# Optimization experiments

Hardware: AMD Instinct MI355X
Metric: run time of the kernel (lower is better)

The kernel has to match this reference:

```python
import jax, jax.numpy as jnp
import numpy as np

ST_RATIO = 1.5  # slice-thickness / in-plane-resolution ratio (module init arg)


def setup_inputs() -> dict:
    key = jax.random.key(0)
    k1, k2 = jax.random.split(key)
    B, H, W, D, S = 8, 160, 160, 96, 64
    vol = jax.random.normal(k1, (B, H, W, D, 1), dtype=jnp.float32)
    # small perturbations around identity (identity row is added inside reference)
    trf = jax.random.normal(k2, (B, S, 12), dtype=jnp.float32) * 0.05
    return {"vol": vol, "trf": trf}


def _trilinear(v, loc):
    """v: [H, W, D] volume; loc: [..., 3] float sample locations (voxel coords).
    Border-clipped trilinear interpolation (as in neuron's interpn)."""
    H, W, D = v.shape
    maxs_f = jnp.asarray([H - 1, W - 1, D - 1], dtype=loc.dtype)
    loc = jnp.clip(loc, 0.0, maxs_f)
    f = jnp.floor(loc)
    d = loc - f  # fractional part, in [0, 1)
    i0 = f.astype(jnp.int32)
    i1 = jnp.minimum(i0 + 1, jnp.asarray([H - 1, W - 1, D - 1], dtype=jnp.int32))
    out = jnp.zeros(loc.shape[:-1], dtype=v.dtype)
    for cx in (0, 1):
        for cy in (0, 1):
            for cz in (0, 1):
                ix = i1[..., 0] if cx else i0[..., 0]
                iy = i1[..., 1] if cy else i0[..., 1]
                iz = i1[..., 2] if cz else i0[..., 2]
                w = ((d[..., 0] if cx else 1.0 - d[..., 0])
                     * (d[..., 1] if cy else 1.0 - d[..., 1])
                     * (d[..., 2] if cz else 1.0 - d[..., 2]))
                out = out + w * v[ix, iy, iz]
    return out


def reference(vol, trf):
    """Volume-to-slice resampling.
    vol: [B, H, W, D, 1]; trf: [B, S, 12] per-slice affine params (flattened 3x4).
    Identity row added per original: trf += eye(4)[:3, :].
    Output: [B, H, W, S, 1]."""
    B, H, W, D, _ = vol.shape
    S = trf.shape[1]
    A = trf.reshape(B, S, 3, 4) + jnp.eye(4, dtype=trf.dtype)[:3, :]  # [B,S,3,4]

    # slice-plane sampling grid: in-plane (i, j) over HxW, through-plane z = s * st_ratio
    ii, jj = jnp.meshgrid(jnp.arange(H, dtype=jnp.float32),
                          jnp.arange(W, dtype=jnp.float32), indexing="ij")
    zz = jnp.arange(S, dtype=jnp.float32) * ST_RATIO
    ones = jnp.ones((S, H, W), dtype=jnp.float32)
    grid = jnp.stack([ii[None] * ones, jj[None] * ones,
                      zz[:, None, None] * ones, ones], axis=-1)  # [S,H,W,4] homogeneous

    loc = jnp.einsum("bsij,shwj->bshwi", A, grid)  # [B,S,H,W,3] volume coords
    out = jax.vmap(_trilinear)(vol[..., 0], loc)    # [B,S,H,W]
    return jnp.transpose(out, (0, 2, 3, 1))[..., None]  # [B,H,W,S,1]
```

## Files before the change

kernel.cpp:

```cpp
#include <hip/hip_runtime.h>
#include <hip/hip_fp16.h>

#define B 8
#define H 160
#define W 160
#define D 96
#define S 64
#define ST_RATIO 1.5f

__global__ __launch_bounds__(256) void v2s_transpose(
    const float* __restrict__ vol, __half* __restrict__ volT)
{
    __shared__ float t[32][33];
    const int blk = blockIdx.x;
    const int bh  = blk / 15;
    const int rem = blk - bh * 15;
    const int wt  = rem / 3;
    const int dt  = rem - wt * 3;
    const float* in  = vol  + (size_t)bh * (W * D);
    __half*      op  = volT + (size_t)bh * (D * W);
    const int tx = threadIdx.x & 31, ty = threadIdx.x >> 5;
#pragma unroll
    for (int r = 0; r < 4; ++r) {
        const int w_ = wt * 32 + ty + 8 * r;
        const int d_ = dt * 32 + tx;
        t[ty + 8 * r][tx] = in[w_ * D + d_];
    }
    __syncthreads();
#pragma unroll
    for (int r = 0; r < 4; ++r) {
        const int d_ = dt * 32 + ty + 8 * r;
        const int w_ = wt * 32 + tx;
        op[d_ * W + w_] = __float2half(t[tx][ty + 8 * r]);
    }
}

__global__ __launch_bounds__(256) void v2s_main(
    const __half* __restrict__ volT,
    const float*  __restrict__ trf,
    float*        __restrict__ out)
{
    __shared__ float As[S * 12];
    __shared__ float outT[64][65];

    const int bid  = blockIdx.x;
    const int tile = (bid & 7) * 400 + (bid >> 3);
    const int b    = tile / 400;
    const int hw0  = (tile - b * 400) * 64;

    const float* tb = trf + (size_t)b * (S * 12);
    for (int e = threadIdx.x; e < S * 12; e += 256) {
        const int j = e % 12;
        float v = tb[e];
        if ((j & 3) == (j >> 2)) v += 1.0f;
        As[e] = v;
    }
    __syncthreads();

    const int lane = threadIdx.x & 63;
    const int wid  = threadIdx.x >> 6;
    const int hw   = hw0 + lane;
    const int h    = hw / W;
    const int w    = hw - h * W;
    const float fh = (float)h, fw = (float)w;
    const __half* vb = volT + (size_t)b * (H * D * W);

#pragma unroll 4
    for (int it = 0; it < 16; ++it) {
        const int s = it * 4 + wid;
        const float* a = &As[s * 12];
        const float fz = (float)s * ST_RATIO;

        float x = fmaf(a[0], fh, fmaf(a[1], fw, fmaf(a[2],  fz, a[3])));
        float y = fmaf(a[4], fh, fmaf(a[5], fw, fmaf(a[6],  fz, a[7])));
        float z = fmaf(a[8], fh, fmaf(a[9], fw, fmaf(a[10], fz, a[11])));

        x = fminf(fmaxf(x, 0.0f), (float)(H - 1));
        y = fminf(fmaxf(y, 0.0f), (float)(W - 1));
        z = fminf(fmaxf(z, 0.0f), (float)(D - 1));

        const float flx = floorf(x), fly = floorf(y), flz = floorf(z);
        const float dx = x - flx, dy = y - fly, dz = z - flz;
        const int ix0 = (int)flx, iy0 = (int)fly, iz0 = (int)flz;
        const int ix1 = min(ix0 + 1, H - 1);
        const int iy1 = min(iy0 + 1, W - 1);
        const int iz1 = min(iz0 + 1, D - 1);

        const __half* p00 = vb + (ix0 * D + iz0) * W;
        const __half* p01 = vb + (ix0 * D + iz1) * W;
        const __half* p10 = vb + (ix1 * D + iz0) * W;
        const __half* p11 = vb + (ix1 * D + iz1) * W;

        const float v000 = __half2float(p00[iy0]), v001 = __half2float(p00[iy1]);
        const float v010 = __half2float(p01[iy0]), v011 = __half2float(p01[iy1]);
        const float v100 = __half2float(p10[iy0]), v101 = __half2float(p10[iy1]);
        const float v110 = __half2float(p11[iy0]), v111 = __half2float(p11[iy1]);

        const float c00 = fmaf(dy, v001 - v000, v000);
        const float c01 = fmaf(dy, v011 - v010, v010);
        const float c10 = fmaf(dy, v101 - v100, v100);
        const float c11 = fmaf(dy, v111 - v110, v110);
        const float c0  = fmaf(dz, c01 - c00, c00);
        const float c1  = fmaf(dz, c11 - c10, c10);
        outT[lane][s]   = fmaf(dx, c1 - c0, c0);
    }
    __syncthreads();

    const int s_out = lane;
#pragma unroll
    for (int r = 0; r < 16; ++r) {
        const int hw_off = wid + 4 * r;
        out[((size_t)(b * (H * W) + hw0 + hw_off)) * S + s_out] = outT[hw_off][s_out];
    }
}

__global__ __launch_bounds__(256) void v2s_fallback(
    const float* __restrict__ vol, const float* __restrict__ trf,
    float* __restrict__ out)
{
    __shared__ float As[S * 13];
    const int pos0 = blockIdx.x * 4;
    const int b = pos0 / (H * W);
    const float* tb = trf + (size_t)b * S * 12;
    for (int e = threadIdx.x; e < S * 12; e += 256) {
        int s = e / 12, j = e - s * 12;
        float v = tb[e];
        if ((j & 3) == (j >> 2)) v += 1.0f;
        As[s * 13 + j] = v;
    }
    __syncthreads();
    const int s   = threadIdx.x & 63;
    const int pos = pos0 + (threadIdx.x >> 6);
    const int hw  = pos % (H * W);
    const int h   = hw / W;
    const int w   = hw - h * W;
    const float* a = &As[s * 13];
    const float fh = (float)h, fw = (float)w, fz = (float)s * ST_RATIO;
    float x = fmaf(a[0], fh, fmaf(a[1], fw, fmaf(a[2],  fz, a[3])));
    float y = fmaf(a[4], fh, fmaf(a[5], fw, fmaf(a[6],  fz, a[7])));
    float z = fmaf(a[8], fh, fmaf(a[9], fw, fmaf(a[10], fz, a[11])));
    x = fminf(fmaxf(x, 0.0f), (float)(H - 1));
    y = fminf(fmaxf(y, 0.0f), (float)(W - 1));
    z = fminf(fmaxf(z, 0.0f), (float)(D - 1));
    const float flx = floorf(x), fly = floorf(y), flz = floorf(z);
    const float dx = x - flx, dy = y - fly, dz = z - flz;
    const int ix0 = (int)flx, iy0 = (int)fly, iz0 = (int)flz;
    const int ix1 = min(ix0 + 1, H - 1);
    const int iy1 = min(iy0 + 1, W - 1);
    const int iz1 = min(iz0 + 1, D - 1);
    const float* vb  = vol + (size_t)b * (H * W * D);
    const float* p00 = vb + (ix0 * W + iy0) * D;
    const float* p01 = vb + (ix0 * W + iy1) * D;
    const float* p10 = vb + (ix1 * W + iy0) * D;
    const float* p11 = vb + (ix1 * W + iy1) * D;
    const float v000 = p00[iz0], v001 = p00[iz1];
    const float v010 = p01[iz0], v011 = p01[iz1];
    const float v100 = p10[iz0], v101 = p10[iz1];
    const float v110 = p11[iz0], v111 = p11[iz1];
    const float c00 = fmaf(dz, v001 - v000, v000);
    const float c01 = fmaf(dz, v011 - v010, v010);
    const float c10 = fmaf(dz, v101 - v100, v100);
    const float c11 = fmaf(dz, v111 - v110, v110);
    const float c0  = fmaf(dy, c01 - c00, c00);
    const float c1  = fmaf(dy, c11 - c10, c10);
    out[(size_t)pos * S + s] = fmaf(dx, c1 - c0, c0);
}

extern "C" void kernel_launch(void* const* d_in, const int* in_sizes, int n_in,
                              void* d_out, int out_size, void* d_ws, size_t ws_size,
                              hipStream_t stream) {
    const float* vol = (const float*)d_in[0];
    const float* trf = (const float*)d_in[1];
    float* out = (float*)d_out;

    const size_t volT_bytes = (size_t)B * H * D * W * sizeof(__half);
    if (ws_size >= volT_bytes) {
        __half* volT = (__half*)d_ws;
        v2s_transpose<<<B * H * 5 * 3, 256, 0, stream>>>(vol, volT);
        v2s_main<<<(B * H * W) / 64, 256, 0, stream>>>(volT, trf, out);
    } else {
        v2s_fallback<<<(B * H * W) / 4, 256, 0, stream>>>(vol, trf, out);
    }
}
```

Before: 188.1 us.

## Pack adjacent-y voxel pairs into half2 so each corner pair needs one load

```diff
diff --git a/kernel.cpp b/kernel.cpp
--- a/kernel.cpp
+++ b/kernel.cpp
@@ -8,37 +8,44 @@
 #define S 64
 #define ST_RATIO 1.5f
 
-__global__ __launch_bounds__(256) void v2s_transpose(
-    const float* __restrict__ vol, __half* __restrict__ volT)
+__global__ __launch_bounds__(256) void v2s_prep3(
+    const float* __restrict__ vol, __half2* __restrict__ volP)
 {
-    __shared__ float t[32][33];
-    const int blk = blockIdx.x;
-    const int bh  = blk / 15;
-    const int rem = blk - bh * 15;
-    const int wt  = rem / 3;
-    const int dt  = rem - wt * 3;
-    const float* in  = vol  + (size_t)bh * (W * D);
-    __half*      op  = volT + (size_t)bh * (D * W);
-    const int tx = threadIdx.x & 31, ty = threadIdx.x >> 5;
-#pragma unroll
-    for (int r = 0; r < 4; ++r) {
-        const int w_ = wt * 32 + ty + 8 * r;
-        const int d_ = dt * 32 + tx;
-        t[ty + 8 * r][tx] = in[w_ * D + d_];
+    __shared__ __half ph[D * 164];
+    const int bh = blockIdx.x;
+    const float* in = vol + (size_t)bh * (W * D);
+
+    for (int i = threadIdx.x; i < W * (D / 4); i += 256) {
+        const int w_ = i / 24, k = i - w_ * 24;
+        const float4 f = *(const float4*)(in + w_ * D + 4 * k);
+        const int d0 = 4 * k;
+        ph[(d0 + 0) * 164 + w_] = __float2half(f.x);
+        ph[(d0 + 1) * 164 + w_] = __float2half(f.y);
+        ph[(d0 + 2) * 164 + w_] = __float2half(f.z);
+        ph[(d0 + 3) * 164 + w_] = __float2half(f.w);
     }
     __syncthreads();
-#pragma unroll
-    for (int r = 0; r < 4; ++r) {
-        const int d_ = dt * 32 + ty + 8 * r;
-        const int w_ = wt * 32 + tx;
-        op[d_ * W + w_] = __float2half(t[tx][ty + 8 * r]);
+
+    __half2* op = volP + (size_t)bh * (D * W);
+    for (int i = threadIdx.x; i < D * (W / 4); i += 256) {
+        const int d = i / 40, g = i - d * 40;
+        const int w0 = 4 * g;
+        const __half* row = &ph[d * 164];
+        const ushort4 a = *(const ushort4*)(row + w0);
+        const unsigned a4 = (unsigned)__half_as_ushort(row[min(w0 + 4, W - 1)]);
+        int4 o;
+        o.x = (int)((unsigned)a.x | ((unsigned)a.y << 16));
+        o.y = (int)((unsigned)a.y | ((unsigned)a.z << 16));
+        o.z = (int)((unsigned)a.z | ((unsigned)a.w << 16));
+        o.w = (int)((unsigned)a.w | (a4 << 16));
+        *(int4*)(op + (size_t)d * W + w0) = o;
     }
 }
 
-__global__ __launch_bounds__(256) void v2s_main(
-    const __half* __restrict__ volT,
-    const float*  __restrict__ trf,
-    float*        __restrict__ out)
+__global__ __launch_bounds__(256) void v2s_main4(
+    const __half2* __restrict__ volP,
+    const float*   __restrict__ trf,
+    float*         __restrict__ out)
 {
     __shared__ float As[S * 12];
     __shared__ float outT[64][65];
@@ -63,7 +70,7 @@
     const int h    = hw / W;
     const int w    = hw - h * W;
     const float fh = (float)h, fw = (float)w;
-    const __half* vb = volT + (size_t)b * (H * D * W);
+    const __half2* vb = volP + (size_t)b * (H * D * W);
 
 #pragma unroll 4
     for (int it = 0; it < 16; ++it) {
@@ -83,23 +90,18 @@
         const float dx = x - flx, dy = y - fly, dz = z - flz;
         const int ix0 = (int)flx, iy0 = (int)fly, iz0 = (int)flz;
         const int ix1 = min(ix0 + 1, H - 1);
-        const int iy1 = min(iy0 + 1, W - 1);
         const int iz1 = min(iz0 + 1, D - 1);
 
-        const __half* p00 = vb + (ix0 * D + iz0) * W;
-        const __half* p01 = vb + (ix0 * D + iz1) * W;
-        const __half* p10 = vb + (ix1 * D + iz0) * W;
-        const __half* p11 = vb + (ix1 * D + iz1) * W;
+        const int r0 = ix0 * D, r1 = ix1 * D;
+        const float2 l00 = __half22float2(vb[(r0 + iz0) * W + iy0]);
+        const float2 l01 = __half22float2(vb[(r0 + iz1) * W + iy0]);
+        const float2 l10 = __half22float2(vb[(r1 + iz0) * W + iy0]);
+        const float2 l11 = __half22float2(vb[(r1 + iz1) * W + iy0]);
 
-        const float v000 = __half2float(p00[iy0]), v001 = __half2float(p00[iy1]);
-        const float v010 = __half2float(p01[iy0]), v011 = __half2float(p01[iy1]);
-        const float v100 = __half2float(p10[iy0]), v101 = __half2float(p10[iy1]);
-        const float v110 = __half2float(p11[iy0]), v111 = __half2float(p11[iy1]);
-
-        const float c00 = fmaf(dy, v001 - v000, v000);
-        const float c01 = fmaf(dy, v011 - v010, v010);
-        const float c10 = fmaf(dy, v101 - v100, v100);
-        const float c11 = fmaf(dy, v111 - v110, v110);
+        const float c00 = fmaf(dy, l00.y - l00.x, l00.x);
+        const float c01 = fmaf(dy, l01.y - l01.x, l01.x);
+        const float c10 = fmaf(dy, l10.y - l10.x, l10.x);
+        const float c11 = fmaf(dy, l11.y - l11.x, l11.x);
         const float c0  = fmaf(dz, c01 - c00, c00);
         const float c1  = fmaf(dz, c11 - c10, c10);
         outT[lane][s]   = fmaf(dx, c1 - c0, c0);
@@ -173,11 +175,11 @@
     const float* trf = (const float*)d_in[1];
     float* out = (float*)d_out;
 
-    const size_t volT_bytes = (size_t)B * H * D * W * sizeof(__half);
-    if (ws_size >= volT_bytes) {
-        __half* volT = (__half*)d_ws;
-        v2s_transpose<<<B * H * 5 * 3, 256, 0, stream>>>(vol, volT);
-        v2s_main<<<(B * H * W) / 64, 256, 0, stream>>>(volT, trf, out);
+    const size_t volP_bytes = (size_t)B * H * D * W * sizeof(__half2);
+    if (ws_size >= volP_bytes) {
+        __half2* volP = (__half2*)d_ws;
+        v2s_prep3<<<B * H, 256, 0, stream>>>(vol, volP);
+        v2s_main4<<<3200, 256, 0, stream>>>(volP, trf, out);
     } else {
         v2s_fallback<<<(B * H * W) / 4, 256, 0, stream>>>(vol, trf, out);
     }
```

Result: faster. 175.2 us (-6.9%).
